# Performance work log

Measured on AMD Instinct MI355X. Metric: run time of the kernel, lower is better.

Reference implementation:

```python
import jax, jax.numpy as jnp
import numpy as np

B, F, Q = 8192, 128, 64
H1, H2 = 256, 256
THRESHOLD = 0.95
EPS = 1e-12


def setup_inputs() -> dict:
    key = jax.random.key(0)
    ks = jax.random.split(key, 8)
    in_dim = F + 1 + Q  # raw + quantum + graph feature
    def lin(k, fan_in, fan_out):
        bound = 1.0 / np.sqrt(fan_in)
        kw, kb = jax.random.split(k)
        W = jax.random.uniform(kw, (fan_out, fan_in), jnp.float32, -bound, bound)
        b = jax.random.uniform(kb, (fan_out,), jnp.float32, -bound, bound)
        return W, b
    W1, b1 = lin(ks[2], in_dim, H1)
    W2, b2 = lin(ks[3], H1, H2)
    W3, b3 = lin(ks[4], H2, 1)
    return {
        'x': jax.random.normal(ks[0], (B, F), jnp.float32),
        'quantum_features': jax.random.normal(ks[1], (B, Q), jnp.float32),
        'W1': W1, 'b1': b1, 'W2': W2, 'b2': b2, 'W3': W3, 'b3': b3,
    }


def _graph_feat(x):
    # normalized Gram matrix -> squared cosine fidelity -> threshold -> row mean
    xn = x / (jnp.linalg.norm(x, axis=1, keepdims=True) + EPS)  # [B, F]
    fid = jnp.square(xn @ xn.T)                                  # [B, B]
    adj = jnp.where(fid >= THRESHOLD, 1.0, 0.0)
    adj = adj * (1.0 - jnp.eye(x.shape[0], dtype=x.dtype))       # no self-edges
    return jnp.mean(adj, axis=1, keepdims=True)                  # [B, 1]


def reference(x, quantum_features, W1, b1, W2, b2, W3, b3):
    graph_feat = jax.lax.stop_gradient(_graph_feat(x))  # built under no_grad in torch
    feats = jnp.concatenate([x, quantum_features, graph_feat], axis=1)  # [B, F+Q+1]
    h = jax.nn.relu(feats @ W1.T + b1)
    h = jax.nn.relu(h @ W2.T + b2)
    out = h @ W3.T + b3  # [B, 1]
    return out[:, 0]
```

## Files before the change

### kernel.cpp

```cpp
#include <hip/hip_runtime.h>
#include <hip/hip_bf16.h>

typedef __attribute__((ext_vector_type(8))) short bf16x8;
typedef __attribute__((ext_vector_type(8))) int i32x8;
typedef __attribute__((ext_vector_type(4))) float f32x4;
typedef unsigned int uint;

#define NROWS 8192
#define F_DIM 128
#define Q_DIM 64
#define KPAD  224
#define H_DIM 256

static __device__ inline unsigned short bf_bits(__hip_bfloat16 b) {
  unsigned short u; __builtin_memcpy(&u, &b, 2); return u;
}
static __device__ inline uint packhl(float v) {
  __hip_bfloat16 h = __float2bfloat16(v);
  float hf = __bfloat162float(h);
  __hip_bfloat16 l = __float2bfloat16(v - hf);
  return ((uint)bf_bits(l) << 16) | (uint)bf_bits(h);
}
static __device__ inline void split_hl(float v, unsigned short& h, unsigned short& l) {
  __hip_bfloat16 hb = __float2bfloat16(v);
  float hf = __bfloat162float(hb);
  __hip_bfloat16 lb = __float2bfloat16(v - hf);
  h = bf_bits(hb); l = bf_bits(lb);
}

union uu { uint4 u; bf16x8 v; };

__global__ __launch_bounds__(256) void norm_prep_kernel(const float* __restrict__ x,
                                                        const float* __restrict__ W1,
                                                        const float* __restrict__ W2,
                                                        unsigned char* __restrict__ xn8,
                                                        uint* __restrict__ W1P,
                                                        uint* __restrict__ W2P,
                                                        int* __restrict__ cnt) {
  int tid = threadIdx.x;
  if (blockIdx.x >= 2048) {
    int b = blockIdx.x - 2048;
    if (b < 256) {
      if (tid < KPAD) W1P[b * KPAD + tid] = (tid < 193) ? packhl(W1[b * 193 + tid]) : 0u;
    } else {
      int n = b - 256;
      W2P[n * 256 + tid] = packhl(W2[n * 256 + tid]);
    }
    return;
  }
  int lane = tid & 63;
  int row = blockIdx.x * 4 + (tid >> 6);
  if (blockIdx.x < 32) cnt[blockIdx.x * 256 + tid] = 0;
  const float2 v = *(const float2*)(x + (size_t)row * F_DIM + lane * 2);
  float s = v.x * v.x + v.y * v.y;
#pragma unroll
  for (int off = 32; off; off >>= 1) s += __shfl_xor(s, off);
  float inv = 1.0f / (sqrtf(s) + 1e-12f);
  int pk = __builtin_amdgcn_cvt_pk_fp8_f32(v.x * inv, v.y * inv, 0, 0);
  *(unsigned short*)(xn8 + (size_t)row * F_DIM + lane * 2) = (unsigned short)(pk & 0xffff);
}

__global__ __launch_bounds__(256) void gram8_kernel(const unsigned char* __restrict__ xn8,
                                                    int* __restrict__ cnt) {
  __shared__ char smem[32768];
  int tid = threadIdx.x;
  int lane = tid & 63;
  int wave = tid >> 6;
  int lr = lane & 15;
  int quad = lane >> 4;

  int t = blockIdx.x;
  int bi = (int)((129.0f - sqrtf(129.0f * 129.0f - 8.0f * (float)t)) * 0.5f);
  while ((bi + 1) * (129 - (bi + 1)) / 2 <= t) bi++;
  while (bi * (129 - bi) / 2 > t) bi--;
  int bj = bi + (t - bi * (129 - bi) / 2);
  int i0 = bi * 128, j0 = bj * 128;

#pragma unroll
  for (int it = 0; it < 8; ++it) {
    int half = it >> 2;
    int row = (it & 3) * 32 + (tid >> 3);
    int chunk = tid & 7;
    int grow = (half ? j0 : i0) + row;
    uint4 v = *(const uint4*)(xn8 + (size_t)grow * F_DIM + chunk * 16);
    *(uint4*)(smem + half * 16384 + row * 128 + ((chunk ^ (row & 7)) << 4)) = v;
  }
  __syncthreads();

  int wi = (wave >> 1) * 64, wj = (wave & 1) * 64;

  f32x4 acc[4][4];
#pragma unroll
  for (int i = 0; i < 4; i++)
#pragma unroll
    for (int j = 0; j < 4; j++) acc[i][j] = (f32x4){0.f, 0.f, 0.f, 0.f};

  i32x8 a[4], b[4];
#pragma unroll
  for (int tt = 0; tt < 4; tt++) {
    int r = wi + tt * 16 + lr;
    const char* base = smem + r * 128;
    uint4 lo = *(const uint4*)(base + (((2 * quad) ^ (r & 7)) << 4));
    uint4 hi = *(const uint4*)(base + (((2 * quad + 1) ^ (r & 7)) << 4));
    i32x8 f;
    f[0] = lo.x; f[1] = lo.y; f[2] = lo.z; f[3] = lo.w;
    f[4] = hi.x; f[5] = hi.y; f[6] = hi.z; f[7] = hi.w;
    a[tt] = f;
  }
#pragma unroll
  for (int tt = 0; tt < 4; tt++) {
    int r = wj + tt * 16 + lr;
    const char* base = smem + 16384 + r * 128;
    uint4 lo = *(const uint4*)(base + (((2 * quad) ^ (r & 7)) << 4));
    uint4 hi = *(const uint4*)(base + (((2 * quad + 1) ^ (r & 7)) << 4));
    i32x8 f;
    f[0] = lo.x; f[1] = lo.y; f[2] = lo.z; f[3] = lo.w;
    f[4] = hi.x; f[5] = hi.y; f[6] = hi.z; f[7] = hi.w;
    b[tt] = f;
  }

#pragma unroll
  for (int tr = 0; tr < 4; tr++)
#pragma unroll
    for (int tc = 0; tc < 4; tc++)
      acc[tr][tc] = __builtin_amdgcn_mfma_scale_f32_16x16x128_f8f6f4(
          a[tr], b[tc], acc[tr][tc], 0, 0, 0, 0x7f7f7f7f, 0, 0x7f7f7f7f);

  int i_base = i0 + wi, j_base = j0 + wj;
  bool diag_wave = (i_base == j_base);
  bool offdiag_block = (bi != bj);

  float mx = 0.f;
#pragma unroll
  for (int tr = 0; tr < 4; tr++)
#pragma unroll
    for (int tc = 0; tc < 4; tc++)
#pragma unroll
      for (int r = 0; r < 4; r++) {
        float v = acc[tr][tc][r];
        if (diag_wave && tr == tc && lr == quad * 4 + r) v = 0.f;
        mx = fmaxf(mx, fabsf(v));
      }
  if (__any(mx >= 0.9746f)) {
    for (int tr = 0; tr < 4; tr++)
      for (int tc = 0; tc < 4; tc++)
        for (int r = 0; r < 4; r++) {
          float v = acc[tr][tc][r];
          int row = i_base + tr * 16 + quad * 4 + r;
          int col = j_base + tc * 16 + lr;
          if (v * v >= 0.95f && row != col) {
            atomicAdd(&cnt[row], 1);
            if (offdiag_block) atomicAdd(&cnt[col], 1);
          }
        }
  }
}

__global__ __launch_bounds__(256) void fused_mlp_kernel(const float* __restrict__ x,
                                                        const float* __restrict__ q,
                                                        const uint* __restrict__ W1P,
                                                        const uint* __restrict__ W2P,
                                                        const float* __restrict__ b1,
                                                        const float* __restrict__ b2,
                                                        const float* __restrict__ W3,
                                                        const float* __restrict__ b3,
                                                        const int* __restrict__ cnt,
                                                        float* __restrict__ out) {
  __shared__ char smem[65536];
  short* Ahs = (short*)smem;
  short* Als = (short*)(smem + 14848);
  uint*  H1  = (uint*)smem;
  uint*  Bx  = (uint*)(smem + 32768);
  float* part = (float*)(smem + 32768);

  int tid = threadIdx.x;
  int lane = tid & 63;
  int wv = tid >> 6;
  int lr = lane & 15;
  int quad = lane >> 4;
  int mb = blockIdx.x * 32;

  {
    int r = tid >> 3;
    int c8 = (tid & 7) * 4;
#pragma unroll
    for (int it = 0; it < 7; ++it) {
      int col = it * 32 + c8;
      float4 v = {0.f, 0.f, 0.f, 0.f};
      if (it < 4)      v = *(const float4*)(x + (size_t)(mb + r) * F_DIM + col);
      else if (it < 6) v = *(const float4*)(q + (size_t)(mb + r) * Q_DIM + (col - 128));
      else if (c8 == 0) v.x = (float)cnt[mb + r] * (1.0f / 8192.0f);
      unsigned short h0, l0, h1, l1, h2, l2, h3, l3;
      split_hl(v.x, h0, l0); split_hl(v.y, h1, l1);
      split_hl(v.z, h2, l2); split_hl(v.w, h3, l3);
      *(uint2*)&Ahs[r * 232 + col] = (uint2){(uint)h0 | ((uint)h1 << 16), (uint)h2 | ((uint)h3 << 16)};
      *(uint2*)&Als[r * 232 + col] = (uint2){(uint)l0 | ((uint)l1 << 16), (uint)l2 | ((uint)l3 << 16)};
    }
  }

  f32x4 acc[2][4];
#pragma unroll
  for (int i = 0; i < 2; i++)
#pragma unroll
    for (int j = 0; j < 4; j++) acc[i][j] = (f32x4){0.f, 0.f, 0.f, 0.f};

  for (int kc = 0; kc < 7; ++kc) {
    int k0 = kc * 32;
    __syncthreads();
#pragma unroll
    for (int i = 0; i < 8; ++i) {
      int flat = i * 256 + tid;
      int n = flat >> 3, j = flat & 7;
      uint4 w = *(const uint4*)(W1P + (size_t)n * KPAD + k0 + j * 4);
      *(uint4*)&Bx[n * 32 + ((j ^ (n & 7)) * 4)] = w;
    }
    __syncthreads();
    bf16x8 ah[2], al[2], bh[4], bl[4];
#pragma unroll
    for (int tt = 0; tt < 2; ++tt) {
      int row = tt * 16 + lr;
      ah[tt] = *(const bf16x8*)&Ahs[row * 232 + k0 + quad * 8];
      al[tt] = *(const bf16x8*)&Als[row * 232 + k0 + quad * 8];
    }
#pragma unroll
    for (int tc = 0; tc < 4; ++tc) {
      int n = wv * 64 + tc * 16 + lr;
      uint4 u0 = *(const uint4*)&Bx[n * 32 + (((quad * 2) ^ (n & 7)) * 4)];
      uint4 u1 = *(const uint4*)&Bx[n * 32 + (((quad * 2 + 1) ^ (n & 7)) * 4)];
      uu h, l;
      h.u.x = (u0.x & 0xffffu) | (u0.y << 16);
      h.u.y = (u0.z & 0xffffu) | (u0.w << 16);
      h.u.z = (u1.x & 0xffffu) | (u1.y << 16);
      h.u.w = (u1.z & 0xffffu) | (u1.w << 16);
      l.u.x = (u0.x >> 16) | (u0.y & 0xffff0000u);
      l.u.y = (u0.z >> 16) | (u0.w & 0xffff0000u);
      l.u.z = (u1.x >> 16) | (u1.y & 0xffff0000u);
      l.u.w = (u1.z >> 16) | (u1.w & 0xffff0000u);
      bh[tc] = h.v; bl[tc] = l.v;
    }
#pragma unroll
    for (int tt = 0; tt < 2; ++tt)
#pragma unroll
      for (int tc = 0; tc < 4; ++tc) {
        acc[tt][tc] = __builtin_amdgcn_mfma_f32_16x16x32_bf16(ah[tt], bh[tc], acc[tt][tc], 0, 0, 0);
        acc[tt][tc] = __builtin_amdgcn_mfma_f32_16x16x32_bf16(ah[tt], bl[tc], acc[tt][tc], 0, 0, 0);
        acc[tt][tc] = __builtin_amdgcn_mfma_f32_16x16x32_bf16(al[tt], bh[tc], acc[tt][tc], 0, 0, 0);
      }
  }

  __syncthreads();
#pragma unroll
  for (int tc = 0; tc < 4; ++tc) {
    int n = wv * 64 + tc * 16 + lr;
    float bv = b1[n];
    int g = n >> 2, jj = n & 3;
#pragma unroll
    for (int tt = 0; tt < 2; ++tt)
#pragma unroll
      for (int r = 0; r < 4; ++r) {
        int row = tt * 16 + quad * 4 + r;
        float v = fmaxf(acc[tt][tc][r] + bv, 0.f);
        H1[row * 256 + ((g ^ (row & 31)) * 4 + jj)] = packhl(v);
      }
  }
#pragma unroll
  for (int i = 0; i < 2; i++)
#pragma unroll
    for (int j = 0; j < 4; j++) acc[i][j] = (f32x4){0.f, 0.f, 0.f, 0.f};

  for (int kc = 0; kc < 8; ++kc) {
    int k0 = kc * 32;
    __syncthreads();
#pragma unroll
    for (int i = 0; i < 8; ++i) {
      int flat = i * 256 + tid;
      int n = flat >> 3, j = flat & 7;
      uint4 w = *(const uint4*)(W2P + (size_t)n * 256 + k0 + j * 4);
      *(uint4*)&Bx[n * 32 + ((j ^ (n & 7)) * 4)] = w;
    }
    __syncthreads();
    bf16x8 ah[2], al[2], bh[4], bl[4];
#pragma unroll
    for (int tt = 0; tt < 2; ++tt) {
      int row = tt * 16 + lr;
      int cb = kc * 8 + quad * 2;
      uint4 u0 = *(const uint4*)&H1[row * 256 + ((cb ^ (row & 31)) * 4)];
      uint4 u1 = *(const uint4*)&H1[row * 256 + (((cb + 1) ^ (row & 31)) * 4)];
      uu h, l;
      h.u.x = (u0.x & 0xffffu) | (u0.y << 16);
      h.u.y = (u0.z & 0xffffu) | (u0.w << 16);
      h.u.z = (u1.x & 0xffffu) | (u1.y << 16);
      h.u.w = (u1.z & 0xffffu) | (u1.w << 16);
      l.u.x = (u0.x >> 16) | (u0.y & 0xffff0000u);
      l.u.y = (u0.z >> 16) | (u0.w & 0xffff0000u);
      l.u.z = (u1.x >> 16) | (u1.y & 0xffff0000u);
      l.u.w = (u1.z >> 16) | (u1.w & 0xffff0000u);
      ah[tt] = h.v; al[tt] = l.v;
    }
#pragma unroll
    for (int tc = 0; tc < 4; ++tc) {
      int n = wv * 64 + tc * 16 + lr;
      uint4 u0 = *(const uint4*)&Bx[n * 32 + (((quad * 2) ^ (n & 7)) * 4)];
      uint4 u1 = *(const uint4*)&Bx[n * 32 + (((quad * 2 + 1) ^ (n & 7)) * 4)];
      uu h, l;
      h.u.x = (u0.x & 0xffffu) | (u0.y << 16);
      h.u.y = (u0.z & 0xffffu) | (u0.w << 16);
      h.u.z = (u1.x & 0xffffu) | (u1.y << 16);
      h.u.w = (u1.z & 0xffffu) | (u1.w << 16);
      l.u.x = (u0.x >> 16) | (u0.y & 0xffff0000u);
      l.u.y = (u0.z >> 16) | (u0.w & 0xffff0000u);
      l.u.z = (u1.x >> 16) | (u1.y & 0xffff0000u);
      l.u.w = (u1.z >> 16) | (u1.w & 0xffff0000u);
      bh[tc] = h.v; bl[tc] = l.v;
    }
#pragma unroll
    for (int tt = 0; tt < 2; ++tt)
#pragma unroll
      for (int tc = 0; tc < 4; ++tc) {
        acc[tt][tc] = __builtin_amdgcn_mfma_f32_16x16x32_bf16(ah[tt], bh[tc], acc[tt][tc], 0, 0, 0);
        acc[tt][tc] = __builtin_amdgcn_mfma_f32_16x16x32_bf16(ah[tt], bl[tc], acc[tt][tc], 0, 0, 0);
        acc[tt][tc] = __builtin_amdgcn_mfma_f32_16x16x32_bf16(al[tt], bh[tc], acc[tt][tc], 0, 0, 0);
      }
  }

  float s[2][4];
#pragma unroll
  for (int tt = 0; tt < 2; ++tt)
#pragma unroll
    for (int r = 0; r < 4; ++r) s[tt][r] = 0.f;
#pragma unroll
  for (int tc = 0; tc < 4; ++tc) {
    int n = wv * 64 + tc * 16 + lr;
    float bv = b2[n];
    float w3 = W3[n];
#pragma unroll
    for (int tt = 0; tt < 2; ++tt)
#pragma unroll
      for (int r = 0; r < 4; ++r)
        s[tt][r] += fmaxf(acc[tt][tc][r] + bv, 0.f) * w3;
  }
#pragma unroll
  for (int tt = 0; tt < 2; ++tt)
#pragma unroll
    for (int r = 0; r < 4; ++r) {
      s[tt][r] += __shfl_xor(s[tt][r], 1);
      s[tt][r] += __shfl_xor(s[tt][r], 2);
      s[tt][r] += __shfl_xor(s[tt][r], 4);
      s[tt][r] += __shfl_xor(s[tt][r], 8);
    }
  __syncthreads();
  if (lr == 0) {
#pragma unroll
    for (int tt = 0; tt < 2; ++tt)
#pragma unroll
      for (int r = 0; r < 4; ++r)
        part[wv * 32 + tt * 16 + quad * 4 + r] = s[tt][r];
  }
  __syncthreads();
  if (tid < 32)
    out[mb + tid] = part[tid] + part[32 + tid] + part[64 + tid] + part[96 + tid] + b3[0];
}

extern "C" void kernel_launch(void* const* d_in, const int* in_sizes, int n_in,
                              void* d_out, int out_size, void* d_ws, size_t ws_size,
                              hipStream_t stream) {
  const float* x  = (const float*)d_in[0];
  const float* q  = (const float*)d_in[1];
  const float* W1 = (const float*)d_in[2];
  const float* b1 = (const float*)d_in[3];
  const float* W2 = (const float*)d_in[4];
  const float* b2 = (const float*)d_in[5];
  const float* W3 = (const float*)d_in[6];
  const float* b3 = (const float*)d_in[7];
  float* out = (float*)d_out;

  char* ws = (char*)d_ws;
  unsigned char* xn8 = (unsigned char*)(ws);
  int*  cnt = (int*)(ws + 0x100000);
  uint* W1P = (uint*)(ws + 0x110000);
  uint* W2P = (uint*)(ws + 0x150000);

  norm_prep_kernel<<<dim3(2560), dim3(256), 0, stream>>>(x, W1, W2, xn8, W1P, W2P, cnt);
  gram8_kernel<<<dim3(2080), dim3(256), 0, stream>>>(xn8, cnt);
  fused_mlp_kernel<<<dim3(256), dim3(256), 0, stream>>>(x, q, W1P, W2P, b1, b2, W3, b3, cnt, out);
}
```

Baseline: 98.68 us.

## Merge three kernels into one cooperative persistent kernel with grid syncs

Replaces the three separate launches (normalize/prep, fp8 Gram count, fused MLP) with one cooperative kernel of 256 blocks that uses grid-wide syncs between phases. The Gram phase becomes a persistent loop over the 2080 upper-triangular tiles, and normalization is vectorized to 8 threads per row. The goal is to remove launch gaps and tail effects between kernels. In exchange it adds grid-sync overhead, and the Gram phase now runs on only 256 blocks with a 64KB shared buffer, so fewer waves are resident to hide latency.

```diff
diff --git a/kernel.cpp b/kernel.cpp
--- a/kernel.cpp
+++ b/kernel.cpp
@@ -1,5 +1,8 @@
 #include <hip/hip_runtime.h>
 #include <hip/hip_bf16.h>
+#include <hip/hip_cooperative_groups.h>
+
+namespace cg = cooperative_groups;
 
 typedef __attribute__((ext_vector_type(8))) short bf16x8;
 typedef __attribute__((ext_vector_type(8))) int i32x8;
@@ -30,335 +33,335 @@
 
 union uu { uint4 u; bf16x8 v; };
 
-__global__ __launch_bounds__(256) void norm_prep_kernel(const float* __restrict__ x,
-                                                        const float* __restrict__ W1,
-                                                        const float* __restrict__ W2,
-                                                        unsigned char* __restrict__ xn8,
-                                                        uint* __restrict__ W1P,
-                                                        uint* __restrict__ W2P,
-                                                        int* __restrict__ cnt) {
+__global__ __launch_bounds__(256, 2) void mega_kernel(const float* __restrict__ x,
+                                                      const float* __restrict__ q,
+                                                      const float* __restrict__ W1,
+                                                      const float* __restrict__ b1,
+                                                      const float* __restrict__ W2,
+                                                      const float* __restrict__ b2,
+                                                      const float* __restrict__ W3,
+                                                      const float* __restrict__ b3,
+                                                      unsigned char* __restrict__ xn8,
+                                                      uint* __restrict__ W1P,
+                                                      uint* __restrict__ W2P,
+                                                      int* __restrict__ cnt,
+                                                      float* __restrict__ out) {
+  __shared__ char smem[65536];
+  cg::grid_group grid = cg::this_grid();
   int tid = threadIdx.x;
-  if (blockIdx.x >= 2048) {
-    int b = blockIdx.x - 2048;
-    if (b < 256) {
-      if (tid < KPAD) W1P[b * KPAD + tid] = (tid < 193) ? packhl(W1[b * 193 + tid]) : 0u;
-    } else {
-      int n = b - 256;
-      W2P[n * 256 + tid] = packhl(W2[n * 256 + tid]);
-    }
-    return;
-  }
-  int lane = tid & 63;
-  int row = blockIdx.x * 4 + (tid >> 6);
-  if (blockIdx.x < 32) cnt[blockIdx.x * 256 + tid] = 0;
-  const float2 v = *(const float2*)(x + (size_t)row * F_DIM + lane * 2);
-  float s = v.x * v.x + v.y * v.y;
-#pragma unroll
-  for (int off = 32; off; off >>= 1) s += __shfl_xor(s, off);
-  float inv = 1.0f / (sqrtf(s) + 1e-12f);
-  int pk = __builtin_amdgcn_cvt_pk_fp8_f32(v.x * inv, v.y * inv, 0, 0);
-  *(unsigned short*)(xn8 + (size_t)row * F_DIM + lane * 2) = (unsigned short)(pk & 0xffff);
-}
-
-__global__ __launch_bounds__(256) void gram8_kernel(const unsigned char* __restrict__ xn8,
-                                                    int* __restrict__ cnt) {
-  __shared__ char smem[32768];
-  int tid = threadIdx.x;
-  int lane = tid & 63;
-  int wave = tid >> 6;
-  int lr = lane & 15;
-  int quad = lane >> 4;
-
-  int t = blockIdx.x;
-  int bi = (int)((129.0f - sqrtf(129.0f * 129.0f - 8.0f * (float)t)) * 0.5f);
-  while ((bi + 1) * (129 - (bi + 1)) / 2 <= t) bi++;
-  while (bi * (129 - bi) / 2 > t) bi--;
-  int bj = bi + (t - bi * (129 - bi) / 2);
-  int i0 = bi * 128, j0 = bj * 128;
-
-#pragma unroll
-  for (int it = 0; it < 8; ++it) {
-    int half = it >> 2;
-    int row = (it & 3) * 32 + (tid >> 3);
-    int chunk = tid & 7;
-    int grow = (half ? j0 : i0) + row;
-    uint4 v = *(const uint4*)(xn8 + (size_t)grow * F_DIM + chunk * 16);
-    *(uint4*)(smem + half * 16384 + row * 128 + ((chunk ^ (row & 7)) << 4)) = v;
-  }
-  __syncthreads();
-
-  int wi = (wave >> 1) * 64, wj = (wave & 1) * 64;
-
-  f32x4 acc[4][4];
-#pragma unroll
-  for (int i = 0; i < 4; i++)
-#pragma unroll
-    for (int j = 0; j < 4; j++) acc[i][j] = (f32x4){0.f, 0.f, 0.f, 0.f};
-
-  i32x8 a[4], b[4];
-#pragma unroll
-  for (int tt = 0; tt < 4; tt++) {
-    int r = wi + tt * 16 + lr;
-    const char* base = smem + r * 128;
-    uint4 lo = *(const uint4*)(base + (((2 * quad) ^ (r & 7)) << 4));
-    uint4 hi = *(const uint4*)(base + (((2 * quad + 1) ^ (r & 7)) << 4));
-    i32x8 f;
-    f[0] = lo.x; f[1] = lo.y; f[2] = lo.z; f[3] = lo.w;
-    f[4] = hi.x; f[5] = hi.y; f[6] = hi.z; f[7] = hi.w;
-    a[tt] = f;
-  }
-#pragma unroll
-  for (int tt = 0; tt < 4; tt++) {
-    int r = wj + tt * 16 + lr;
-    const char* base = smem + 16384 + r * 128;
-    uint4 lo = *(const uint4*)(base + (((2 * quad) ^ (r & 7)) << 4));
-    uint4 hi = *(const uint4*)(base + (((2 * quad + 1) ^ (r & 7)) << 4));
-    i32x8 f;
-    f[0] = lo.x; f[1] = lo.y; f[2] = lo.z; f[3] = lo.w;
-    f[4] = hi.x; f[5] = hi.y; f[6] = hi.z; f[7] = hi.w;
-    b[tt] = f;
-  }
-
-#pragma unroll
-  for (int tr = 0; tr < 4; tr++)
-#pragma unroll
-    for (int tc = 0; tc < 4; tc++)
-      acc[tr][tc] = __builtin_amdgcn_mfma_scale_f32_16x16x128_f8f6f4(
-          a[tr], b[tc], acc[tr][tc], 0, 0, 0, 0x7f7f7f7f, 0, 0x7f7f7f7f);
-
-  int i_base = i0 + wi, j_base = j0 + wj;
-  bool diag_wave = (i_base == j_base);
-  bool offdiag_block = (bi != bj);
-
-  float mx = 0.f;
-#pragma unroll
-  for (int tr = 0; tr < 4; tr++)
-#pragma unroll
-    for (int tc = 0; tc < 4; tc++)
-#pragma unroll
-      for (int r = 0; r < 4; r++) {
-        float v = acc[tr][tc][r];
-        if (diag_wave && tr == tc && lr == quad * 4 + r) v = 0.f;
-        mx = fmaxf(mx, fabsf(v));
-      }
-  if (__any(mx >= 0.9746f)) {
-    for (int tr = 0; tr < 4; tr++)
-      for (int tc = 0; tc < 4; tc++)
-        for (int r = 0; r < 4; r++) {
-          float v = acc[tr][tc][r];
-          int row = i_base + tr * 16 + quad * 4 + r;
-          int col = j_base + tc * 16 + lr;
-          if (v * v >= 0.95f && row != col) {
-            atomicAdd(&cnt[row], 1);
-            if (offdiag_block) atomicAdd(&cnt[col], 1);
-          }
-        }
-  }
-}
-
-__global__ __launch_bounds__(256) void fused_mlp_kernel(const float* __restrict__ x,
-                                                        const float* __restrict__ q,
-                                                        const uint* __restrict__ W1P,
-                                                        const uint* __restrict__ W2P,
-                                                        const float* __restrict__ b1,
-                                                        const float* __restrict__ b2,
-                                                        const float* __restrict__ W3,
-                                                        const float* __restrict__ b3,
-                                                        const int* __restrict__ cnt,
-                                                        float* __restrict__ out) {
-  __shared__ char smem[65536];
-  short* Ahs = (short*)smem;
-  short* Als = (short*)(smem + 14848);
-  uint*  H1  = (uint*)smem;
-  uint*  Bx  = (uint*)(smem + 32768);
-  float* part = (float*)(smem + 32768);
-
-  int tid = threadIdx.x;
+  int bid = blockIdx.x;
   int lane = tid & 63;
   int wv = tid >> 6;
   int lr = lane & 15;
   int quad = lane >> 4;
-  int mb = blockIdx.x * 32;
 
   {
-    int r = tid >> 3;
-    int c8 = (tid & 7) * 4;
-#pragma unroll
-    for (int it = 0; it < 7; ++it) {
-      int col = it * 32 + c8;
-      float4 v = {0.f, 0.f, 0.f, 0.f};
-      if (it < 4)      v = *(const float4*)(x + (size_t)(mb + r) * F_DIM + col);
-      else if (it < 6) v = *(const float4*)(q + (size_t)(mb + r) * Q_DIM + (col - 128));
-      else if (c8 == 0) v.x = (float)cnt[mb + r] * (1.0f / 8192.0f);
-      unsigned short h0, l0, h1, l1, h2, l2, h3, l3;
-      split_hl(v.x, h0, l0); split_hl(v.y, h1, l1);
-      split_hl(v.z, h2, l2); split_hl(v.w, h3, l3);
-      *(uint2*)&Ahs[r * 232 + col] = (uint2){(uint)h0 | ((uint)h1 << 16), (uint)h2 | ((uint)h3 << 16)};
-      *(uint2*)&Als[r * 232 + col] = (uint2){(uint)l0 | ((uint)l1 << 16), (uint)l2 | ((uint)l3 << 16)};
-    }
+    int row = bid * 32 + (tid >> 3);
+    int sub = tid & 7;
+    const float4* xp = (const float4*)(x + (size_t)row * F_DIM) + sub * 4;
+    float4 v0 = xp[0], v1 = xp[1], v2 = xp[2], v3 = xp[3];
+    float s = v0.x * v0.x + v0.y * v0.y + v0.z * v0.z + v0.w * v0.w
+            + v1.x * v1.x + v1.y * v1.y + v1.z * v1.z + v1.w * v1.w
+            + v2.x * v2.x + v2.y * v2.y + v2.z * v2.z + v2.w * v2.w
+            + v3.x * v3.x + v3.y * v3.y + v3.z * v3.z + v3.w * v3.w;
+    s += __shfl_xor(s, 1); s += __shfl_xor(s, 2); s += __shfl_xor(s, 4);
+    float inv = 1.0f / (sqrtf(s) + 1e-12f);
+    int w0 = __builtin_amdgcn_cvt_pk_fp8_f32(v0.x * inv, v0.y * inv, 0, 0);
+    w0 = __builtin_amdgcn_cvt_pk_fp8_f32(v0.z * inv, v0.w * inv, w0, 1);
+    int w1 = __builtin_amdgcn_cvt_pk_fp8_f32(v1.x * inv, v1.y * inv, 0, 0);
+    w1 = __builtin_amdgcn_cvt_pk_fp8_f32(v1.z * inv, v1.w * inv, w1, 1);
+    int w2 = __builtin_amdgcn_cvt_pk_fp8_f32(v2.x * inv, v2.y * inv, 0, 0);
+    w2 = __builtin_amdgcn_cvt_pk_fp8_f32(v2.z * inv, v2.w * inv, w2, 1);
+    int w3 = __builtin_amdgcn_cvt_pk_fp8_f32(v3.x * inv, v3.y * inv, 0, 0);
+    w3 = __builtin_amdgcn_cvt_pk_fp8_f32(v3.z * inv, v3.w * inv, w3, 1);
+    uint4 pk; pk.x = (uint)w0; pk.y = (uint)w1; pk.z = (uint)w2; pk.w = (uint)w3;
+    *(uint4*)(xn8 + (size_t)row * F_DIM + sub * 16) = pk;
+
+    if (tid < KPAD) W1P[bid * KPAD + tid] = (tid < 193) ? packhl(W1[bid * 193 + tid]) : 0u;
+    W2P[bid * 256 + tid] = packhl(W2[bid * 256 + tid]);
+    if (bid < 32) cnt[bid * 256 + tid] = 0;
   }
 
-  f32x4 acc[2][4];
-#pragma unroll
-  for (int i = 0; i < 2; i++)
-#pragma unroll
-    for (int j = 0; j < 4; j++) acc[i][j] = (f32x4){0.f, 0.f, 0.f, 0.f};
-
-  for (int kc = 0; kc < 7; ++kc) {
-    int k0 = kc * 32;
-    __syncthreads();
-#pragma unroll
-    for (int i = 0; i < 8; ++i) {
-      int flat = i * 256 + tid;
-      int n = flat >> 3, j = flat & 7;
-      uint4 w = *(const uint4*)(W1P + (size_t)n * KPAD + k0 + j * 4);
-      *(uint4*)&Bx[n * 32 + ((j ^ (n & 7)) * 4)] = w;
-    }
-    __syncthreads();
-    bf16x8 ah[2], al[2], bh[4], bl[4];
-#pragma unroll
-    for (int tt = 0; tt < 2; ++tt) {
-      int row = tt * 16 + lr;
-      ah[tt] = *(const bf16x8*)&Ahs[row * 232 + k0 + quad * 8];
-      al[tt] = *(const bf16x8*)&Als[row * 232 + k0 + quad * 8];
-    }
+  grid.sync();
+
+  for (int t = bid; t < 2080; t += 256) {
+    int bi = (int)((129.0f - sqrtf(129.0f * 129.0f - 8.0f * (float)t)) * 0.5f);
+    while ((bi + 1) * (129 - (bi + 1)) / 2 <= t) bi++;
+    while (bi * (129 - bi) / 2 > t) bi--;
+    int bj = bi + (t - bi * (129 - bi) / 2);
+    int i0 = bi * 128, j0 = bj * 128;
+
+    __syncthreads();
+#pragma unroll
+    for (int it = 0; it < 8; ++it) {
+      int half = it >> 2;
+      int row = (it & 3) * 32 + (tid >> 3);
+      int chunk = tid & 7;
+      int grow = (half ? j0 : i0) + row;
+      uint4 v = *(const uint4*)(xn8 + (size_t)grow * F_DIM + chunk * 16);
+      *(uint4*)(smem + half * 16384 + row * 128 + ((chunk ^ (row & 7)) << 4)) = v;
+    }
+    __syncthreads();
+
+    int wi = (wv >> 1) * 64, wj = (wv & 1) * 64;
+
+    i32x8 a[4], b[4];
+#pragma unroll
+    for (int tt = 0; tt < 4; tt++) {
+      int r = wi + tt * 16 + lr;
+      const char* base = smem + r * 128;
+      uint4 lo = *(const uint4*)(base + (((2 * quad) ^ (r & 7)) << 4));
+      uint4 hi = *(const uint4*)(base + (((2 * quad + 1) ^ (r & 7)) << 4));
+      i32x8 f;
+      f[0] = lo.x; f[1] = lo.y; f[2] = lo.z; f[3] = lo.w;
+      f[4] = hi.x; f[5] = hi.y; f[6] = hi.z; f[7] = hi.w;
+      a[tt] = f;
+    }
+#pragma unroll
+    for (int tt = 0; tt < 4; tt++) {
+      int r = wj + tt * 16 + lr;
+      const char* base = smem + 16384 + r * 128;
+      uint4 lo = *(const uint4*)(base + (((2 * quad) ^ (r & 7)) << 4));
+      uint4 hi = *(const uint4*)(base + (((2 * quad + 1) ^ (r & 7)) << 4));
+      i32x8 f;
+      f[0] = lo.x; f[1] = lo.y; f[2] = lo.z; f[3] = lo.w;
+      f[4] = hi.x; f[5] = hi.y; f[6] = hi.z; f[7] = hi.w;
+      b[tt] = f;
+    }
+
+    f32x4 acc[4][4];
+#pragma unroll
+    for (int i = 0; i < 4; i++)
+#pragma unroll
+      for (int j = 0; j < 4; j++) acc[i][j] = (f32x4){0.f, 0.f, 0.f, 0.f};
+
+#pragma unroll
+    for (int tr = 0; tr < 4; tr++)
+#pragma unroll
+      for (int tc = 0; tc < 4; tc++)
+        acc[tr][tc] = __builtin_amdgcn_mfma_scale_f32_16x16x128_f8f6f4(
+            a[tr], b[tc], acc[tr][tc], 0, 0, 0, 0x7f7f7f7f, 0, 0x7f7f7f7f);
+
+    int i_base = i0 + wi, j_base = j0 + wj;
+    bool diag_wave = (i_base == j_base);
+    bool offdiag_block = (bi != bj);
+
+    float mx = 0.f;
+#pragma unroll
+    for (int tr = 0; tr < 4; tr++)
+#pragma unroll
+      for (int tc = 0; tc < 4; tc++)
+#pragma unroll
+        for (int r = 0; r < 4; r++) {
+          float v = acc[tr][tc][r];
+          if (diag_wave && tr == tc && lr == quad * 4 + r) v = 0.f;
+          mx = fmaxf(mx, fabsf(v));
+        }
+    if (__any(mx >= 0.9746f)) {
+      for (int tr = 0; tr < 4; tr++)
+        for (int tc = 0; tc < 4; tc++)
+          for (int r = 0; r < 4; r++) {
+            float v = acc[tr][tc][r];
+            int row = i_base + tr * 16 + quad * 4 + r;
+            int col = j_base + tc * 16 + lr;
+            if (v * v >= 0.95f && row != col) {
+              atomicAdd(&cnt[row], 1);
+              if (offdiag_block) atomicAdd(&cnt[col], 1);
+            }
+          }
+    }
+  }
+
+  grid.sync();
+
+  {
+    short* Ahs = (short*)smem;
+    short* Als = (short*)(smem + 14848);
+    uint*  H1  = (uint*)smem;
+    uint*  Bx  = (uint*)(smem + 32768);
+    float* part = (float*)(smem + 32768);
+    int mb = bid * 32;
+
+    {
+      int r = tid >> 3;
+      int c8 = (tid & 7) * 4;
+#pragma unroll
+      for (int it = 0; it < 7; ++it) {
+        int col = it * 32 + c8;
+        float4 v = {0.f, 0.f, 0.f, 0.f};
+        if (it < 4)      v = *(const float4*)(x + (size_t)(mb + r) * F_DIM + col);
+        else if (it < 6) v = *(const float4*)(q + (size_t)(mb + r) * Q_DIM + (col - 128));
+        else if (c8 == 0) v.x = (float)cnt[mb + r] * (1.0f / 8192.0f);
+        unsigned short h0, l0, h1, l1, h2, l2, h3, l3;
+        split_hl(v.x, h0, l0); split_hl(v.y, h1, l1);
+        split_hl(v.z, h2, l2); split_hl(v.w, h3, l3);
+        *(uint2*)&Ahs[r * 232 + col] = (uint2){(uint)h0 | ((uint)h1 << 16), (uint)h2 | ((uint)h3 << 16)};
+        *(uint2*)&Als[r * 232 + col] = (uint2){(uint)l0 | ((uint)l1 << 16), (uint)l2 | ((uint)l3 << 16)};
+      }
+    }
+
+    f32x4 acc[2][4];
+#pragma unroll
+    for (int i = 0; i < 2; i++)
+#pragma unroll
+      for (int j = 0; j < 4; j++) acc[i][j] = (f32x4){0.f, 0.f, 0.f, 0.f};
+
+    for (int kc = 0; kc < 7; ++kc) {
+      int k0 = kc * 32;
+      __syncthreads();
+#pragma unroll
+      for (int i = 0; i < 8; ++i) {
+        int flat = i * 256 + tid;
+        int n = flat >> 3, j = flat & 7;
+        uint4 w = *(const uint4*)(W1P + (size_t)n * KPAD + k0 + j * 4);
+        *(uint4*)&Bx[n * 32 + ((j ^ (n & 7)) * 4)] = w;
+      }
+      __syncthreads();
+      bf16x8 ah[2], al[2], bh[4], bl[4];
+#pragma unroll
+      for (int tt = 0; tt < 2; ++tt) {
+        int row = tt * 16 + lr;
+        ah[tt] = *(const bf16x8*)&Ahs[row * 232 + k0 + quad * 8];
+        al[tt] = *(const bf16x8*)&Als[row * 232 + k0 + quad * 8];
+      }
+#pragma unroll
+      for (int tc = 0; tc < 4; ++tc) {
+        int n = wv * 64 + tc * 16 + lr;
+        uint4 u0 = *(const uint4*)&Bx[n * 32 + (((quad * 2) ^ (n & 7)) * 4)];
+        uint4 u1 = *(const uint4*)&Bx[n * 32 + (((quad * 2 + 1) ^ (n & 7)) * 4)];
+        uu h, l;
+        h.u.x = (u0.x & 0xffffu) | (u0.y << 16);
+        h.u.y = (u0.z & 0xffffu) | (u0.w << 16);
+        h.u.z = (u1.x & 0xffffu) | (u1.y << 16);
+        h.u.w = (u1.z & 0xffffu) | (u1.w << 16);
+        l.u.x = (u0.x >> 16) | (u0.y & 0xffff0000u);
+        l.u.y = (u0.z >> 16) | (u0.w & 0xffff0000u);
+        l.u.z = (u1.x >> 16) | (u1.y & 0xffff0000u);
+        l.u.w = (u1.z >> 16) | (u1.w & 0xffff0000u);
+        bh[tc] = h.v; bl[tc] = l.v;
+      }
+#pragma unroll
+      for (int tt = 0; tt < 2; ++tt)
+#pragma unroll
+        for (int tc = 0; tc < 4; ++tc) {
+          acc[tt][tc] = __builtin_amdgcn_mfma_f32_16x16x32_bf16(ah[tt], bh[tc], acc[tt][tc], 0, 0, 0);
+          acc[tt][tc] = __builtin_amdgcn_mfma_f32_16x16x32_bf16(ah[tt], bl[tc], acc[tt][tc], 0, 0, 0);
+          acc[tt][tc] = __builtin_amdgcn_mfma_f32_16x16x32_bf16(al[tt], bh[tc], acc[tt][tc], 0, 0, 0);
+        }
+    }
+
+    __syncthreads();
 #pragma unroll
     for (int tc = 0; tc < 4; ++tc) {
       int n = wv * 64 + tc * 16 + lr;
-      uint4 u0 = *(const uint4*)&Bx[n * 32 + (((quad * 2) ^ (n & 7)) * 4)];
-      uint4 u1 = *(const uint4*)&Bx[n * 32 + (((quad * 2 + 1) ^ (n & 7)) * 4)];
-      uu h, l;
-      h.u.x = (u0.x & 0xffffu) | (u0.y << 16);
-      h.u.y = (u0.z & 0xffffu) | (u0.w << 16);
-      h.u.z = (u1.x & 0xffffu) | (u1.y << 16);
-      h.u.w = (u1.z & 0xffffu) | (u1.w << 16);
-      l.u.x = (u0.x >> 16) | (u0.y & 0xffff0000u);
-      l.u.y = (u0.z >> 16) | (u0.w & 0xffff0000u);
-      l.u.z = (u1.x >> 16) | (u1.y & 0xffff0000u);
-      l.u.w = (u1.z >> 16) | (u1.w & 0xffff0000u);
-      bh[tc] = h.v; bl[tc] = l.v;
-    }
+      float bv = b1[n];
+      int g = n >> 2, jj = n & 3;
+#pragma unroll
+      for (int tt = 0; tt < 2; ++tt)
+#pragma unroll
+        for (int r = 0; r < 4; ++r) {
+          int row = tt * 16 + quad * 4 + r;
+          float v = fmaxf(acc[tt][tc][r] + bv, 0.f);
+          H1[row * 256 + ((g ^ (row & 31)) * 4 + jj)] = packhl(v);
+        }
+    }
+#pragma unroll
+    for (int i = 0; i < 2; i++)
+#pragma unroll
+      for (int j = 0; j < 4; j++) acc[i][j] = (f32x4){0.f, 0.f, 0.f, 0.f};
+
+    for (int kc = 0; kc < 8; ++kc) {
+      int k0 = kc * 32;
+      __syncthreads();
+#pragma unroll
+      for (int i = 0; i < 8; ++i) {
+        int flat = i * 256 + tid;
+        int n = flat >> 3, j = flat & 7;
+        uint4 w = *(const uint4*)(W2P + (size_t)n * 256 + k0 + j * 4);
+        *(uint4*)&Bx[n * 32 + ((j ^ (n & 7)) * 4)] = w;
+      }
+      __syncthreads();
+      bf16x8 ah[2], al[2], bh[4], bl[4];
+#pragma unroll
+      for (int tt = 0; tt < 2; ++tt) {
+        int row = tt * 16 + lr;
+        int cb = kc * 8 + quad * 2;
+        uint4 u0 = *(const uint4*)&H1[row * 256 + ((cb ^ (row & 31)) * 4)];
+        uint4 u1 = *(const uint4*)&H1[row * 256 + (((cb + 1) ^ (row & 31)) * 4)];
+        uu h, l;
+        h.u.x = (u0.x & 0xffffu) | (u0.y << 16);
+        h.u.y = (u0.z & 0xffffu) | (u0.w << 16);
+        h.u.z = (u1.x & 0xffffu) | (u1.y << 16);
+        h.u.w = (u1.z & 0xffffu) | (u1.w << 16);
+        l.u.x = (u0.x >> 16) | (u0.y & 0xffff0000u);
+        l.u.y = (u0.z >> 16) | (u0.w & 0xffff0000u);
+        l.u.z = (u1.x >> 16) | (u1.y & 0xffff0000u);
+        l.u.w = (u1.z >> 16) | (u1.w & 0xffff0000u);
+        ah[tt] = h.v; al[tt] = l.v;
+      }
+#pragma unroll
+      for (int tc = 0; tc < 4; ++tc) {
+        int n = wv * 64 + tc * 16 + lr;
+        uint4 u0 = *(const uint4*)&Bx[n * 32 + (((quad * 2) ^ (n & 7)) * 4)];
+        uint4 u1 = *(const uint4*)&Bx[n * 32 + (((quad * 2 + 1) ^ (n & 7)) * 4)];
+        uu h, l;
+        h.u.x = (u0.x & 0xffffu) | (u0.y << 16);
+        h.u.y = (u0.z & 0xffffu) | (u0.w << 16);
+        h.u.z = (u1.x & 0xffffu) | (u1.y << 16);
+        h.u.w = (u1.z & 0xffffu) | (u1.w << 16);
+        l.u.x = (u0.x >> 16) | (u0.y & 0xffff0000u);
+        l.u.y = (u0.z >> 16) | (u0.w & 0xffff0000u);
+        l.u.z = (u1.x >> 16) | (u1.y & 0xffff0000u);
+        l.u.w = (u1.z >> 16) | (u1.w & 0xffff0000u);
+        bh[tc] = h.v; bl[tc] = l.v;
+      }
+#pragma unroll
+      for (int tt = 0; tt < 2; ++tt)
+#pragma unroll
+        for (int tc = 0; tc < 4; ++tc) {
+          acc[tt][tc] = __builtin_amdgcn_mfma_f32_16x16x32_bf16(ah[tt], bh[tc], acc[tt][tc], 0, 0, 0);
+          acc[tt][tc] = __builtin_amdgcn_mfma_f32_16x16x32_bf16(ah[tt], bl[tc], acc[tt][tc], 0, 0, 0);
+          acc[tt][tc] = __builtin_amdgcn_mfma_f32_16x16x32_bf16(al[tt], bh[tc], acc[tt][tc], 0, 0, 0);
+        }
+    }
+
+    float s[2][4];
 #pragma unroll
     for (int tt = 0; tt < 2; ++tt)
 #pragma unroll
-      for (int tc = 0; tc < 4; ++tc) {
-        acc[tt][tc] = __builtin_amdgcn_mfma_f32_16x16x32_bf16(ah[tt], bh[tc], acc[tt][tc], 0, 0, 0);
-        acc[tt][tc] = __builtin_amdgcn_mfma_f32_16x16x32_bf16(ah[tt], bl[tc], acc[tt][tc], 0, 0, 0);
-        acc[tt][tc] = __builtin_amdgcn_mfma_f32_16x16x32_bf16(al[tt], bh[tc], acc[tt][tc], 0, 0, 0);
-      }
-  }
-
-  __syncthreads();
-#pragma unroll
-  for (int tc = 0; tc < 4; ++tc) {
-    int n = wv * 64 + tc * 16 + lr;
-    float bv = b1[n];
-    int g = n >> 2, jj = n & 3;
-#pragma unroll
-    for (int tt = 0; tt < 2; ++tt)
-#pragma unroll
-      for (int r = 0; r < 4; ++r) {
-        int row = tt * 16 + quad * 4 + r;
-        float v = fmaxf(acc[tt][tc][r] + bv, 0.f);
-        H1[row * 256 + ((g ^ (row & 31)) * 4 + jj)] = packhl(v);
-      }
-  }
-#pragma unroll
-  for (int i = 0; i < 2; i++)
-#pragma unroll
-    for (int j = 0; j < 4; j++) acc[i][j] = (f32x4){0.f, 0.f, 0.f, 0.f};
-
-  for (int kc = 0; kc < 8; ++kc) {
-    int k0 = kc * 32;
-    __syncthreads();
-#pragma unroll
-    for (int i = 0; i < 8; ++i) {
-      int flat = i * 256 + tid;
-      int n = flat >> 3, j = flat & 7;
-      uint4 w = *(const uint4*)(W2P + (size_t)n * 256 + k0 + j * 4);
-      *(uint4*)&Bx[n * 32 + ((j ^ (n & 7)) * 4)] = w;
-    }
-    __syncthreads();
-    bf16x8 ah[2], al[2], bh[4], bl[4];
-#pragma unroll
-    for (int tt = 0; tt < 2; ++tt) {
-      int row = tt * 16 + lr;
-      int cb = kc * 8 + quad * 2;
-      uint4 u0 = *(const uint4*)&H1[row * 256 + ((cb ^ (row & 31)) * 4)];
-      uint4 u1 = *(const uint4*)&H1[row * 256 + (((cb + 1) ^ (row & 31)) * 4)];
-      uu h, l;
-      h.u.x = (u0.x & 0xffffu) | (u0.y << 16);
-      h.u.y = (u0.z & 0xffffu) | (u0.w << 16);
-      h.u.z = (u1.x & 0xffffu) | (u1.y << 16);
-      h.u.w = (u1.z & 0xffffu) | (u1.w << 16);
-      l.u.x = (u0.x >> 16) | (u0.y & 0xffff0000u);
-      l.u.y = (u0.z >> 16) | (u0.w & 0xffff0000u);
-      l.u.z = (u1.x >> 16) | (u1.y & 0xffff0000u);
-      l.u.w = (u1.z >> 16) | (u1.w & 0xffff0000u);
-      ah[tt] = h.v; al[tt] = l.v;
-    }
+      for (int r = 0; r < 4; ++r) s[tt][r] = 0.f;
 #pragma unroll
     for (int tc = 0; tc < 4; ++tc) {
       int n = wv * 64 + tc * 16 + lr;
-      uint4 u0 = *(const uint4*)&Bx[n * 32 + (((quad * 2) ^ (n & 7)) * 4)];
-      uint4 u1 = *(const uint4*)&Bx[n * 32 + (((quad * 2 + 1) ^ (n & 7)) * 4)];
-      uu h, l;
-      h.u.x = (u0.x & 0xffffu) | (u0.y << 16);
-      h.u.y = (u0.z & 0xffffu) | (u0.w << 16);
-      h.u.z = (u1.x & 0xffffu) | (u1.y << 16);
-      h.u.w = (u1.z & 0xffffu) | (u1.w << 16);
-      l.u.x = (u0.x >> 16) | (u0.y & 0xffff0000u);
-      l.u.y = (u0.z >> 16) | (u0.w & 0xffff0000u);
-      l.u.z = (u1.x >> 16) | (u1.y & 0xffff0000u);
-      l.u.w = (u1.z >> 16) | (u1.w & 0xffff0000u);
-      bh[tc] = h.v; bl[tc] = l.v;
+      float bv = b2[n];
+      float w3 = W3[n];
+#pragma unroll
+      for (int tt = 0; tt < 2; ++tt)
+#pragma unroll
+        for (int r = 0; r < 4; ++r)
+          s[tt][r] += fmaxf(acc[tt][tc][r] + bv, 0.f) * w3;
     }
 #pragma unroll
     for (int tt = 0; tt < 2; ++tt)
 #pragma unroll
-      for (int tc = 0; tc < 4; ++tc) {
-        acc[tt][tc] = __builtin_amdgcn_mfma_f32_16x16x32_bf16(ah[tt], bh[tc], acc[tt][tc], 0, 0, 0);
-        acc[tt][tc] = __builtin_amdgcn_mfma_f32_16x16x32_bf16(ah[tt], bl[tc], acc[tt][tc], 0, 0, 0);
-        acc[tt][tc] = __builtin_amdgcn_mfma_f32_16x16x32_bf16(al[tt], bh[tc], acc[tt][tc], 0, 0, 0);
-      }
+      for (int r = 0; r < 4; ++r) {
+        s[tt][r] += __shfl_xor(s[tt][r], 1);
+        s[tt][r] += __shfl_xor(s[tt][r], 2);
+        s[tt][r] += __shfl_xor(s[tt][r], 4);
+        s[tt][r] += __shfl_xor(s[tt][r], 8);
+      }
+    __syncthreads();
+    if (lr == 0) {
+#pragma unroll
+      for (int tt = 0; tt < 2; ++tt)
+#pragma unroll
+        for (int r = 0; r < 4; ++r)
+          part[wv * 32 + tt * 16 + quad * 4 + r] = s[tt][r];
+    }
+    __syncthreads();
+    if (tid < 32)
+      out[mb + tid] = part[tid] + part[32 + tid] + part[64 + tid] + part[96 + tid] + b3[0];
   }
-
-  float s[2][4];
-#pragma unroll
-  for (int tt = 0; tt < 2; ++tt)
-#pragma unroll
-    for (int r = 0; r < 4; ++r) s[tt][r] = 0.f;
-#pragma unroll
-  for (int tc = 0; tc < 4; ++tc) {
-    int n = wv * 64 + tc * 16 + lr;
-    float bv = b2[n];
-    float w3 = W3[n];
-#pragma unroll
-    for (int tt = 0; tt < 2; ++tt)
-#pragma unroll
-      for (int r = 0; r < 4; ++r)
-        s[tt][r] += fmaxf(acc[tt][tc][r] + bv, 0.f) * w3;
-  }
-#pragma unroll
-  for (int tt = 0; tt < 2; ++tt)
-#pragma unroll
-    for (int r = 0; r < 4; ++r) {
-      s[tt][r] += __shfl_xor(s[tt][r], 1);
-      s[tt][r] += __shfl_xor(s[tt][r], 2);
-      s[tt][r] += __shfl_xor(s[tt][r], 4);
-      s[tt][r] += __shfl_xor(s[tt][r], 8);
-    }
-  __syncthreads();
-  if (lr == 0) {
-#pragma unroll
-    for (int tt = 0; tt < 2; ++tt)
-#pragma unroll
-      for (int r = 0; r < 4; ++r)
-        part[wv * 32 + tt * 16 + quad * 4 + r] = s[tt][r];
-  }
-  __syncthreads();
-  if (tid < 32)
-    out[mb + tid] = part[tid] + part[32 + tid] + part[64 + tid] + part[96 + tid] + b3[0];
 }
 
 extern "C" void kernel_launch(void* const* d_in, const int* in_sizes, int n_in,
@@ -380,7 +383,8 @@
   uint* W1P = (uint*)(ws + 0x110000);
   uint* W2P = (uint*)(ws + 0x150000);
 
-  norm_prep_kernel<<<dim3(2560), dim3(256), 0, stream>>>(x, W1, W2, xn8, W1P, W2P, cnt);
-  gram8_kernel<<<dim3(2080), dim3(256), 0, stream>>>(xn8, cnt);
-  fused_mlp_kernel<<<dim3(256), dim3(256), 0, stream>>>(x, q, W1P, W2P, b1, b2, W3, b3, cnt, out);
-}
+  void* args[] = {(void*)&x, (void*)&q, (void*)&W1, (void*)&b1, (void*)&W2, (void*)&b2,
+                  (void*)&W3, (void*)&b3, (void*)&xn8, (void*)&W1P, (void*)&W2P,
+                  (void*)&cnt, (void*)&out};
+  hipLaunchCooperativeKernel((void*)mega_kernel, dim3(256), dim3(256), args, 0, stream);
+}
```

Measured after the change: 174.3 us. 76.6% more time.
